# Kernel optimization log

Hardware: AMD Instinct MI355X
Metric: run time of the kernel (lower is better)

The kernel has to match this reference:

```python
import jax, jax.numpy as jnp
import numpy as np

NT, NF, CIN, COUT = 1_500_000, 500_000, 32, 32
BN_EPS = 1e-5


def setup_inputs() -> dict:
    key = jax.random.key(0)
    k1, k2, k3 = jax.random.split(key, 3)
    input_texture = jax.random.normal(k1, (NT, CIN), dtype=jnp.float32)
    # barycentric coefficients: nonnegative, rows sum to 1
    b = jax.random.uniform(k2, (NT, 3), dtype=jnp.float32) + 1e-3
    bary_coeff = b / b.sum(axis=1, keepdims=True)
    # 3 texture samples per facet (sum == NT)
    num_texture = jnp.full((NF,), 3, dtype=jnp.int32)
    # xavier-normal init for [Cout, Cin, 3] kernel
    fan = CIN * 3 + COUT * 3
    std = float(np.sqrt(2.0 / fan))
    weights = jax.random.normal(k3, (COUT, CIN, 3), dtype=jnp.float32) * std
    bias = jnp.zeros((1, COUT), dtype=jnp.float32)
    gamma = jnp.ones((COUT,), dtype=jnp.float32)
    beta = jnp.zeros((COUT,), dtype=jnp.float32)
    return {"input_texture": input_texture, "bary_coeff": bary_coeff,
            "num_texture": num_texture, "weights": weights, "bias": bias,
            "gamma": gamma, "beta": beta}


def reference(input_texture, bary_coeff, num_texture, weights, bias, gamma, beta):
    nf = num_texture.shape[0]
    nt = input_texture.shape[0]
    # segment id for each ragged texture sample (original op uses cumsum offsets)
    seg = jnp.repeat(jnp.arange(nf), num_texture, total_repeat_length=nt)
    # per-sample contribution: y[t,o] = sum_{c,k} x[t,c] * b[t,k] * W[o,c,k]
    y = jnp.einsum('tc,tk,ock->to', input_texture, bary_coeff, weights)
    # facet2facet averages over the samples of each facet
    s = jax.ops.segment_sum(y, seg, num_segments=nf)  # [Nf, Cout]
    cnt = jnp.maximum(num_texture.astype(y.dtype), 1)[:, None]
    out = s / cnt
    out = out + bias          # bias add
    out = jax.nn.relu(out)    # activation
    # BatchNorm1d in training mode: batch statistics over the facet dim
    mean = out.mean(axis=0)
    var = out.var(axis=0)
    out = (out - mean) * jax.lax.rsqrt(var + BN_EPS) * gamma + beta
    return out
```

## Files before the change

kernel.cpp:

```cpp
#include <hip/hip_runtime.h>
#include <hip/hip_bf16.h>
#include <stdint.h>

typedef __attribute__((ext_vector_type(4))) float fv4;
typedef __attribute__((ext_vector_type(4))) short sv4;
typedef __attribute__((ext_vector_type(8))) short sv8;

typedef __attribute__((address_space(3))) float lds_f;
typedef __attribute__((address_space(1))) const float glb_f;

#define SCHUNK 2048
#define NIT 8
#define SPAN (4 * NIT * 16)

static __device__ __forceinline__ short f2bf(float f) {
  __hip_bfloat16 h = __float2bfloat16(f);
  union { __hip_bfloat16 h; short s; } u; u.h = h;
  return u.s;
}

__global__ __launch_bounds__(256) void scan1(const int* __restrict__ num, int nf,
                                             int* __restrict__ bsum) {
  __shared__ int sd[256];
  int b = blockIdx.x, tid = threadIdx.x;
  int base = b * SCHUNK + tid * 8;
  int s = 0;
#pragma unroll
  for (int j = 0; j < 8; ++j) { int i = base + j; if (i < nf) s += num[i]; }
  sd[tid] = s; __syncthreads();
  for (int st = 128; st > 0; st >>= 1) {
    if (tid < st) sd[tid] += sd[tid + st];
    __syncthreads();
  }
  if (tid == 0) bsum[b] = sd[0];
}

__global__ __launch_bounds__(256) void scan2(int* __restrict__ bsum, int nb) {
  __shared__ int sd[256];
  int tid = threadIdx.x;
  int v = (tid < nb) ? bsum[tid] : 0;
  sd[tid] = v; __syncthreads();
  for (int off = 1; off < 256; off <<= 1) {
    int t = (tid >= off) ? sd[tid - off] : 0;
    __syncthreads();
    sd[tid] += t;
    __syncthreads();
  }
  if (tid < nb) bsum[tid] = sd[tid] - v;
}

__global__ __launch_bounds__(256) void scan3(const int* __restrict__ num, int nf,
                                             const int* __restrict__ bsum,
                                             int* __restrict__ offsets) {
  __shared__ int sc_[256];
  int b = blockIdx.x, tid = threadIdx.x;
  int base = b * SCHUNK + tid * 8;
  int loc[8]; int s = 0;
#pragma unroll
  for (int j = 0; j < 8; ++j) {
    loc[j] = (base + j < nf) ? num[base + j] : 0;
    s += loc[j];
  }
  sc_[tid] = s; __syncthreads();
  for (int off = 1; off < 256; off <<= 1) {
    int t = (tid >= off) ? sc_[tid - off] : 0;
    __syncthreads();
    sc_[tid] += t;
    __syncthreads();
  }
  int run = bsum[b] + sc_[tid] - s;
#pragma unroll
  for (int j = 0; j < 8; ++j) {
    if (base + j < nf) offsets[base + j] = run;
    run += loc[j];
  }
  if (b == gridDim.x - 1 && tid == 255) offsets[nf] = run;
}

__global__ __launch_bounds__(256) void k_prep(const float* __restrict__ W,
                                              short* __restrict__ w2g) {
  for (int i = threadIdx.x; i < 3072; i += 256) {
    int o = i / 96;
    int ck = i - o * 96;
    int k = ck >> 5, c = ck & 31;
    w2g[o * 96 + ck] = f2bf(W[o * 96 + c * 3 + k]);
  }
}

#define WAITN_(N) do { \
  asm volatile("s_waitcnt vmcnt(" #N ")" ::: "memory"); \
  __builtin_amdgcn_sched_barrier(0); \
} while (0)
#define WAITN(N) WAITN_(N)

#define STAGE(T, BUF) do { \
  if (can_stage) { \
    const int f0t_ = blk0w + (T) * 16; \
    long r0_ = 3L * f0t_; \
    long br_ = (r0_ + 48 <= (long)nt) ? r0_ : (long)nt - 48; \
    const float* gx_ = x + br_ * 32; \
    float* lb_ = &Xs[wv][BUF][0]; \
    _Pragma("unroll") \
    for (int i_ = 0; i_ < 6; ++i_) { \
      int L_ = i_ * 64 + lane; \
      int G_ = L_ ^ ((L_ >> 3) & 7); \
      __builtin_amdgcn_global_load_lds((glb_f*)(gx_ + G_ * 4), (lds_f*)(lb_ + i_ * 256), 16, 0, 0); \
    } \
    const float* gb_ = bary + br_ * 3; \
    if (lane < 36) \
      __builtin_amdgcn_global_load_lds((glb_f*)(gb_ + lane * 4), (lds_f*)(&Bs[wv][BUF][0]), 16, 0, 0); \
  } \
} while (0)

#define LOADR(S, T) do { \
  const int f_ = blk0w + (T) * 16 + rowl; \
  const int fa_ = f_ < nf ? f_ : nf; \
  const int fb_ = (f_ + 1) < nf ? (f_ + 1) : nf; \
  st_##S = offsets[fa_]; \
  en_##S = offsets[fb_]; \
} while (0)

#define PART(S, T, BUF, STG, WN) do { \
  WAITN(WN); \
  const int f0t = blk0w + (T) * 16; \
  const int f_ = f0t + rowl; \
  const int nm_my = en_##S - st_##S; \
  const bool dense_ = can_stage && (3L * f0t + 48 <= (long)nt); \
  const bool dense_st = (f0t + 16 <= nf); \
  float z0[8], z1[8], z2[8]; \
  _Pragma("unroll") \
  for (int j = 0; j < 8; ++j) { z0[j] = 0.f; z1[j] = 0.f; z2[j] = 0.f; } \
  if (dense_ && nm_my == 3 && st_##S == 3 * f_) { \
    const float* Xb_ = &Xs[wv][BUF][0]; \
    const float* bb_ = &Bs[wv][BUF][9 * rowl]; \
    _Pragma("unroll") \
    for (int s_ = 0; s_ < 3; ++s_) { \
      int row_ = 3 * rowl + s_; \
      int sw_ = row_ & 7; \
      fv4 xa = *(const fv4*)(Xb_ + (((row_ * 8 + grp) ^ sw_) << 2)); \
      fv4 xb = *(const fv4*)(Xb_ + (((row_ * 8 + 4 + grp) ^ sw_) << 2)); \
      float b0_ = bb_[3 * s_ + 0]; \
      float b1_ = bb_[3 * s_ + 1]; \
      float b2_ = bb_[3 * s_ + 2]; \
      _Pragma("unroll") \
      for (int j = 0; j < 4; ++j) { \
        z0[j]     += xa[j] * b0_; z1[j]     += xa[j] * b1_; z2[j]     += xa[j] * b2_; \
        z0[4 + j] += xb[j] * b0_; z1[4 + j] += xb[j] * b1_; z2[4 + j] += xb[j] * b2_; \
      } \
    } \
  } else { \
    for (int t2 = st_##S; t2 < en_##S; ++t2) { \
      const float* xp = x + (size_t)t2 * 32; \
      fv4 xa = *(const fv4*)(xp + cb_lo); \
      fv4 xb = *(const fv4*)(xp + cb_hi); \
      const float* bpp = bary + (size_t)t2 * 3; \
      float b0_ = bpp[0], b1_ = bpp[1], b2_ = bpp[2]; \
      _Pragma("unroll") \
      for (int j = 0; j < 4; ++j) { \
        z0[j]     += xa[j] * b0_; z1[j]     += xa[j] * b1_; z2[j]     += xa[j] * b2_; \
        z0[4 + j] += xb[j] * b0_; z1[4 + j] += xb[j] * b1_; z2[4 + j] += xb[j] * b2_; \
      } \
    } \
  } \
  fv4 acc0 = (fv4){0.f, 0.f, 0.f, 0.f}; \
  fv4 acc1 = (fv4){0.f, 0.f, 0.f, 0.f}; \
  _Pragma("unroll") \
  for (int kb = 0; kb < 3; ++kb) { \
    sv8 afr; \
    _Pragma("unroll") \
    for (int j = 0; j < 4; ++j) { \
      float lo = (kb == 0) ? z0[j]     : (kb == 1) ? z1[j]     : z2[j]; \
      float hi = (kb == 0) ? z0[4 + j] : (kb == 1) ? z1[4 + j] : z2[4 + j]; \
      afr[j]     = f2bf(lo); \
      afr[4 + j] = f2bf(hi); \
    } \
    acc0 = __builtin_amdgcn_mfma_f32_16x16x32_bf16(afr, bfrA[kb], acc0, 0, 0, 0); \
    acc1 = __builtin_amdgcn_mfma_f32_16x16x32_bf16(afr, bfrB[kb], acc1, 0, 0, 0); \
  } \
  float* yw = &Yt[wv][0]; \
  _Pragma("unroll") \
  for (int r = 0; r < 4; ++r) { \
    int row = grp * 4 + r; \
    int fr = f0t + row; \
    int nm = __shfl(nm_my, row, 64); \
    float inv = 1.0f / (float)(nm > 1 ? nm : 1); \
    float v0 = fmaxf(acc0[r] * inv + bo0, 0.f); \
    float v1 = fmaxf(acc1[r] * inv + bo1, 0.f); \
    if (dense_st) { \
      yw[row * 32 + rowl]      = v0; \
      yw[row * 32 + 16 + rowl] = v1; \
      s1l += v0; s2l += v0 * v0; \
      s1h += v1; s2h += v1 * v1; \
    } else if (fr < nf) { \
      out[fr * 32 + rowl]      = v0; \
      out[fr * 32 + 16 + rowl] = v1; \
      s1l += v0; s2l += v0 * v0; \
      s1h += v1; s2h += v1 * v1; \
    } \
  } \
  if (dense_st) { \
    __builtin_amdgcn_wave_barrier(); \
    const float* yr = &Yt[wv][0]; \
    fv4 o0 = *(const fv4*)(yr + lane * 4); \
    fv4 o1 = *(const fv4*)(yr + 256 + lane * 4); \
    float* op = out + (size_t)f0t * 32; \
    *(fv4*)(op + lane * 4)       = o0; \
    *(fv4*)(op + 256 + lane * 4) = o1; \
    __builtin_amdgcn_wave_barrier(); \
  } \
  if (STG) { \
    __builtin_amdgcn_sched_barrier(0); \
    STAGE((T) + 2, BUF); \
    LOADR(S, (T) + 2); \
  } \
} while (0)

__global__ __launch_bounds__(256, 2) void k_main(
    const float* __restrict__ x, const float* __restrict__ bary,
    const short* __restrict__ w2g, const float* __restrict__ bias,
    const int* __restrict__ offsets, float* __restrict__ out,
    float* __restrict__ partials, int nf, int nt, int nw)
{
  __shared__ __align__(16) float Xs[4][2][1536];
  __shared__ __align__(16) float Bs[4][2][256];
  __shared__ __align__(16) float Yt[4][512];

  const int tid = threadIdx.x;
  const int lane = tid & 63;
  const int wv = tid >> 6;

  const int rowl = lane & 15;
  const int grp = lane >> 4;
  const int cb_lo = grp * 4;
  const int cb_hi = grp * 4 + 16;
  const int blk0w = blockIdx.x * SPAN + wv * (NIT * 16);

  sv8 bfrA[3], bfrB[3];
#pragma unroll
  for (int kb = 0; kb < 3; ++kb) {
    const int cko = kb * 32 + grp * 4;
    {
      const short* wr = w2g + rowl * 96 + cko;
      sv4 lo = *(const sv4*)(wr), hi = *(const sv4*)(wr + 16);
#pragma unroll
      for (int j = 0; j < 4; ++j) { bfrA[kb][j] = lo[j]; bfrA[kb][4 + j] = hi[j]; }
    }
    {
      const short* wr = w2g + (16 + rowl) * 96 + cko;
      sv4 lo = *(const sv4*)(wr), hi = *(const sv4*)(wr + 16);
#pragma unroll
      for (int j = 0; j < 4; ++j) { bfrB[kb][j] = lo[j]; bfrB[kb][4 + j] = hi[j]; }
    }
  }

  float bo0 = bias[rowl];
  float bo1 = bias[16 + rowl];
  float s1l = 0.f, s1h = 0.f, s2l = 0.f, s2h = 0.f;

  const bool can_stage = (nt >= 48);

  int st_A, en_A, st_B, en_B;

  STAGE(0, 0);
  LOADR(A, 0);
  STAGE(1, 1);
  LOADR(B, 1);

  for (int t = 0; t < NIT - 2; t += 2) {
    PART(A, t, 0, 1, 11);
    PART(B, t + 1, 1, 1, 11);
  }
  PART(A, NIT - 2, 0, 0, 11);
  PART(B, NIT - 1, 1, 0, 2);

  s1l += __shfl_xor(s1l, 16, 64); s1l += __shfl_xor(s1l, 32, 64);
  s1h += __shfl_xor(s1h, 16, 64); s1h += __shfl_xor(s1h, 32, 64);
  s2l += __shfl_xor(s2l, 16, 64); s2l += __shfl_xor(s2l, 32, 64);
  s2h += __shfl_xor(s2h, 16, 64); s2h += __shfl_xor(s2h, 32, 64);
  if (grp == 0) {
    int w = blockIdx.x * 4 + wv;
    partials[(long)(rowl)      * nw + w] = s1l;
    partials[(long)(16 + rowl) * nw + w] = s1h;
    partials[(long)(32 + rowl) * nw + w] = s2l;
    partials[(long)(48 + rowl) * nw + w] = s2h;
  }
}

__global__ __launch_bounds__(256) void k_reduce(const float* __restrict__ partials,
                                                int nw, float* __restrict__ stats) {
  __shared__ float sd[256];
  int c = blockIdx.x;
  const float* p = partials + (long)c * nw;
  float s = 0.f;
  for (int i = threadIdx.x; i < nw; i += 256) s += p[i];
  sd[threadIdx.x] = s; __syncthreads();
  for (int st = 128; st > 0; st >>= 1) {
    if (threadIdx.x < st) sd[threadIdx.x] += sd[threadIdx.x + st];
    __syncthreads();
  }
  if (threadIdx.x == 0) stats[c] = sd[0];
}

__global__ __launch_bounds__(256) void k_bn(float* __restrict__ out,
                                            const float* __restrict__ stats,
                                            const float* __restrict__ gamma,
                                            const float* __restrict__ beta, int nf) {
  __shared__ float sc[32], sh[32];
  if (threadIdx.x < 32) {
    int o = threadIdx.x;
    float inv_n = 1.0f / (float)nf;
    float mean = stats[o] * inv_n;
    float var = stats[32 + o] * inv_n - mean * mean;
    float rstd = rsqrtf(var + 1e-5f);
    float g = gamma[o] * rstd;
    sc[o] = g;
    sh[o] = beta[o] - mean * g;
  }
  __syncthreads();
  long total4 = (long)nf * 8;
  long idx0 = (long)blockIdx.x * 256 + threadIdx.x;
  int ob = ((int)idx0 & 7) * 4;
  fv4 scv = *(const fv4*)&sc[ob];
  fv4 shv = *(const fv4*)&sh[ob];
  for (long idx = idx0; idx < total4; idx += (long)gridDim.x * 256) {
    fv4 v = *((const fv4*)out + idx);
    v = v * scv + shv;
    *((fv4*)out + idx) = v;
  }
}

extern "C" void kernel_launch(void* const* d_in, const int* in_sizes, int n_in,
                              void* d_out, int out_size, void* d_ws, size_t ws_size,
                              hipStream_t stream) {
  const float* x     = (const float*)d_in[0];
  const float* bary  = (const float*)d_in[1];
  const int*   numt  = (const int*)d_in[2];
  const float* W     = (const float*)d_in[3];
  const float* bias  = (const float*)d_in[4];
  const float* gamma = (const float*)d_in[5];
  const float* beta  = (const float*)d_in[6];
  float* out = (float*)d_out;

  const int nf   = in_sizes[2];
  const int nt   = in_sizes[0] / 32;
  const int nblk = (nf + SPAN - 1) / SPAN;
  const int nw   = nblk * 4;
  const int nbS  = (nf + SCHUNK - 1) / SCHUNK;

  char* w = (char*)d_ws;
  int* offsets = (int*)w;
  size_t off1 = (4UL * (size_t)(nf + 1) + 255) & ~255UL;
  int* bsum = (int*)(w + off1);
  size_t off2 = (off1 + 4UL * (size_t)nbS + 255) & ~255UL;
  short* w2g = (short*)(w + off2);
  size_t off3 = (off2 + 2UL * 3072UL + 255) & ~255UL;
  float* partials = (float*)(w + off3);
  size_t off4 = (off3 + 4UL * 64UL * (size_t)nw + 255) & ~255UL;
  float* stats = (float*)(w + off4);

  scan1<<<nbS, 256, 0, stream>>>(numt, nf, bsum);
  scan2<<<1, 256, 0, stream>>>(bsum, nbS);
  scan3<<<nbS, 256, 0, stream>>>(numt, nf, bsum, offsets);
  k_prep<<<1, 256, 0, stream>>>(W, w2g);
  k_main<<<nblk, 256, 0, stream>>>(x, bary, w2g, bias, offsets, out, partials, nf, nt, nw);
  k_reduce<<<64, 256, 0, stream>>>(partials, nw, stats);
  k_bn<<<2048, 256, 0, stream>>>(out, stats, gamma, beta, nf);
}
```

Baseline: 96.22 us.

## Deepen per-wave pipeline to four stages with two-wave blocks

Reshapes k_main into 128-thread blocks of two waves, each wave handling 16 tiles instead of 8, and widens the per-wave LDS staging ring from two to four buffers. Prefetch now runs four tiles ahead with four register load sets (A-D), and the wait counts are adjusted to match. The aim is to keep more global loads in flight per wave and hide memory latency better. In exchange it uses more LDS and registers per wave, which can lower occupancy, and it relies on the hand-tuned vmcnt wait values being correct.

Result: slower. 102.1 us (+6.1%).

```diff
diff --git a/kernel.cpp b/kernel.cpp
--- a/kernel.cpp
+++ b/kernel.cpp
@@ -10,8 +10,9 @@
 typedef __attribute__((address_space(1))) const float glb_f;
 
 #define SCHUNK 2048
-#define NIT 8
-#define SPAN (4 * NIT * 16)
+#define NIT 16
+#define NWV 2
+#define SPAN (NWV * NIT * 16)
 
 static __device__ __forceinline__ short f2bf(float f) {
   __hip_bfloat16 h = __float2bfloat16(f);
@@ -210,20 +211,20 @@
   } \
   if (STG) { \
     __builtin_amdgcn_sched_barrier(0); \
-    STAGE((T) + 2, BUF); \
-    LOADR(S, (T) + 2); \
+    STAGE((T) + 4, BUF); \
+    LOADR(S, (T) + 4); \
   } \
 } while (0)
 
-__global__ __launch_bounds__(256, 2) void k_main(
+__global__ __launch_bounds__(128) void k_main(
     const float* __restrict__ x, const float* __restrict__ bary,
     const short* __restrict__ w2g, const float* __restrict__ bias,
     const int* __restrict__ offsets, float* __restrict__ out,
     float* __restrict__ partials, int nf, int nt, int nw)
 {
-  __shared__ __align__(16) float Xs[4][2][1536];
-  __shared__ __align__(16) float Bs[4][2][256];
-  __shared__ __align__(16) float Yt[4][512];
+  __shared__ __align__(16) float Xs[NWV][4][1536];
+  __shared__ __align__(16) float Bs[NWV][4][256];
+  __shared__ __align__(16) float Yt[NWV][512];
 
   const int tid = threadIdx.x;
   const int lane = tid & 63;
@@ -259,26 +260,35 @@
 
   const bool can_stage = (nt >= 48);
 
-  int st_A, en_A, st_B, en_B;
-
-  STAGE(0, 0);
-  LOADR(A, 0);
-  STAGE(1, 1);
-  LOADR(B, 1);
-
-  for (int t = 0; t < NIT - 2; t += 2) {
-    PART(A, t, 0, 1, 11);
-    PART(B, t + 1, 1, 1, 11);
-  }
-  PART(A, NIT - 2, 0, 0, 11);
-  PART(B, NIT - 1, 1, 0, 2);
+  int st_A, en_A, st_B, en_B, st_C, en_C, st_D, en_D;
+
+  STAGE(0, 0); LOADR(A, 0);
+  STAGE(1, 1); LOADR(B, 1);
+  STAGE(2, 2); LOADR(C, 2);
+  STAGE(3, 3); LOADR(D, 3);
+
+  PART(A, 0, 0, 1, 21);
+  PART(B, 1, 1, 1, 21);
+  PART(C, 2, 2, 1, 21);
+  PART(D, 3, 3, 1, 21);
+#pragma unroll
+  for (int t = 4; t < NIT - 4; t += 4) {
+    PART(A, t, 0, 1, 27);
+    PART(B, t + 1, 1, 1, 27);
+    PART(C, t + 2, 2, 1, 27);
+    PART(D, t + 3, 3, 1, 27);
+  }
+  PART(A, NIT - 4, 0, 0, 27);
+  PART(B, NIT - 3, 1, 0, 20);
+  PART(C, NIT - 2, 2, 0, 13);
+  PART(D, NIT - 1, 3, 0, 6);
 
   s1l += __shfl_xor(s1l, 16, 64); s1l += __shfl_xor(s1l, 32, 64);
   s1h += __shfl_xor(s1h, 16, 64); s1h += __shfl_xor(s1h, 32, 64);
   s2l += __shfl_xor(s2l, 16, 64); s2l += __shfl_xor(s2l, 32, 64);
   s2h += __shfl_xor(s2h, 16, 64); s2h += __shfl_xor(s2h, 32, 64);
   if (grp == 0) {
-    int w = blockIdx.x * 4 + wv;
+    int w = blockIdx.x * NWV + wv;
     partials[(long)(rowl)      * nw + w] = s1l;
     partials[(long)(16 + rowl) * nw + w] = s1h;
     partials[(long)(32 + rowl) * nw + w] = s2l;
@@ -344,7 +354,7 @@
   const int nf   = in_sizes[2];
   const int nt   = in_sizes[0] / 32;
   const int nblk = (nf + SPAN - 1) / SPAN;
-  const int nw   = nblk * 4;
+  const int nw   = nblk * NWV;
   const int nbS  = (nf + SCHUNK - 1) / SCHUNK;
 
   char* w = (char*)d_ws;
@@ -362,7 +372,7 @@
   scan2<<<1, 256, 0, stream>>>(bsum, nbS);
   scan3<<<nbS, 256, 0, stream>>>(numt, nf, bsum, offsets);
   k_prep<<<1, 256, 0, stream>>>(W, w2g);
-  k_main<<<nblk, 256, 0, stream>>>(x, bary, w2g, bias, offsets, out, partials, nf, nt, nw);
+  k_main<<<nblk, NWV * 64, 0, stream>>>(x, bary, w2g, bias, offsets, out, partials, nf, nt, nw);
   k_reduce<<<64, 256, 0, stream>>>(partials, nw, stats);
   k_bn<<<2048, 256, 0, stream>>>(out, stats, gamma, beta, nf);
 }
```
